# Performance work log

Measured on AMD Instinct MI355X. Metric: run time of the kernel, lower is better.

## Reference

```python
import jax, jax.numpy as jnp
import numpy as np

D_MODEL, D_STATE, D_CONV, EXPAND, HEADDIM = 256, 16, 4, 2, 16
D_INNER = EXPAND * D_MODEL            # 512
NHEADS = D_INNER // HEADDIM           # 32
CONV_DIM = D_INNER + 2 * D_STATE      # 544 (ngroups=1)
D_IN_PROJ = 2 * D_INNER + 2 * D_STATE + NHEADS  # 1088
BATCH, SEQLEN = 8, 4096


def setup_inputs() -> dict:
    key = jax.random.key(0)
    ks = jax.random.split(key, 8)
    u = jax.random.normal(ks[0], (BATCH, SEQLEN, D_MODEL), jnp.float32)
    W_in = jax.random.normal(ks[1], (D_MODEL, D_IN_PROJ), jnp.float32) * 0.02
    conv_w = jax.random.normal(ks[2], (CONV_DIM, 1, D_CONV), jnp.float32) * 0.2
    conv_b = jnp.zeros((CONV_DIM,), jnp.float32)
    # dt_bias init: inverse-softplus of dt ~ Uniform in log-space [dt_min, dt_max]
    dt = jnp.exp(jax.random.uniform(ks[3], (NHEADS,), jnp.float32)
                 * (np.log(0.1) - np.log(0.001)) + np.log(0.001))
    dt = jnp.clip(dt, 1e-4, None)
    dt_bias = dt + jnp.log(-jnp.expm1(-dt))
    A_log = jnp.log(jax.random.uniform(ks[4], (NHEADS,), jnp.float32, 1.0, 16.0))
    D = jnp.ones((NHEADS,), jnp.float32)
    norm_w = jnp.ones((D_INNER,), jnp.float32)
    W_out = jax.random.normal(ks[5], (D_INNER, D_MODEL), jnp.float32) * 0.02
    return dict(u=u, W_in=W_in, conv_w=conv_w, conv_b=conv_b, dt_bias=dt_bias,
                A_log=A_log, D=D, norm_w=norm_w, W_out=W_out)


def _mamba2_forward(u, W_in, conv_w, conv_b, dt_bias, A_log, D, norm_w, W_out):
    batch, seqlen, _ = u.shape
    zxbcdt = u @ W_in                                   # (B, L, 2*d_inner + 2*N + H)
    z = zxbcdt[..., :D_INNER]                           # gate
    xBC = zxbcdt[..., D_INNER:2 * D_INNER + 2 * D_STATE]
    dt = jax.nn.softplus(zxbcdt[..., -NHEADS:] + dt_bias)  # (B, L, H)
    # causal depthwise conv1d over time + SiLU
    xc = jnp.transpose(xBC, (0, 2, 1))                  # (B, C, L)
    xc = jax.lax.conv_general_dilated(
        xc, conv_w, window_strides=(1,), padding=[(D_CONV - 1, 0)],
        feature_group_count=CONV_DIM, dimension_numbers=('NCH', 'OIH', 'NCH'))
    xBC = jax.nn.silu(jnp.transpose(xc, (0, 2, 1)) + conv_b)
    x = xBC[..., :D_INNER].reshape(batch, seqlen, NHEADS, HEADDIM)  # (B,L,H,P)
    Bm = xBC[..., D_INNER:D_INNER + D_STATE]            # (B, L, N), ngroups=1
    Cm = xBC[..., D_INNER + D_STATE:]                   # (B, L, N)
    A = -jnp.exp(A_log)                                 # (H,)
    dA = jnp.exp(dt * A)                                # (B, L, H) decay per step

    # selective scan: h_t = dA_t * h_{t-1} + dt_t * (B_t outer x_t); y_t = C_t . h_t
    def step(h, inp):
        da_t, dt_t, b_t, x_t, c_t = inp
        h = da_t[:, :, None, None] * h + jnp.einsum('bh,bn,bhp->bhpn', dt_t, b_t, x_t)
        y_t = jnp.einsum('bhpn,bn->bhp', h, c_t)
        return h, y_t

    h0 = jnp.zeros((batch, NHEADS, HEADDIM, D_STATE), u.dtype)
    xs = (jnp.moveaxis(dA, 1, 0), jnp.moveaxis(dt, 1, 0),
          jnp.moveaxis(Bm, 1, 0), jnp.moveaxis(x, 1, 0), jnp.moveaxis(Cm, 1, 0))
    _, ys = jax.lax.scan(step, h0, xs)                  # ys: (L, B, H, P)
    y = jnp.moveaxis(ys, 0, 1) + D[None, None, :, None] * x
    y = y.reshape(batch, seqlen, D_INNER)
    # gated RMSNorm (norm_before_gate=False): normalize(y * silu(z)) * weight
    t = y * jax.nn.silu(z)
    t = t * jax.lax.rsqrt(jnp.mean(t * t, axis=-1, keepdims=True) + 1e-5) * norm_w
    return t @ W_out


def reference(u, W_in, conv_w, conv_b, dt_bias, A_log, D, norm_w, W_out):
    return _mamba2_forward(u, W_in, conv_w, conv_b, dt_bias, A_log, D, norm_w, W_out)
```

## Files before the change

### kernel.cpp

```cpp
#include <hip/hip_runtime.h>
#include <hip/hip_bf16.h>
#include <math.h>

#define BATCH   8
#define SEQLEN  4096
#define DMODEL  256
#define DSTATE  16
#define NHEADS  32
#define HEADDIM 16
#define DINNER  512
#define CONVDIM 544
#define DINPROJ 1088
#define NROWS   (BATCH*SEQLEN)
#define CHUNK   64
#define NCH     (SEQLEN/CHUNK)

typedef __attribute__((ext_vector_type(8))) short short8;
typedef __attribute__((ext_vector_type(8))) unsigned short ushort8;
typedef __attribute__((ext_vector_type(4))) float f32x4;

__device__ __forceinline__ float bfu2f(unsigned short u){
  union { float f; unsigned int i; } x; x.i = ((unsigned int)u) << 16; return x.f;
}
__device__ __forceinline__ unsigned short f2bfu(float f){
  union { float f; unsigned int u; } v; v.f = f;
  v.u += 0x7fffu + ((v.u >> 16) & 1u);
  return (unsigned short)(v.u >> 16);
}

__global__ __launch_bounds__(256) void k_cast_u(const float* __restrict__ u, unsigned short* __restrict__ ub){
  int i = blockIdx.x*256 + threadIdx.x;
  float4 v = reinterpret_cast<const float4*>(u)[i];
  ushort4 o; o.x=f2bfu(v.x); o.y=f2bfu(v.y); o.z=f2bfu(v.z); o.w=f2bfu(v.w);
  reinterpret_cast<ushort4*>(ub)[i] = o;
}

__global__ __launch_bounds__(256) void k_transpose_cast(const float* __restrict__ W, unsigned short* __restrict__ WT, int K, int N){
  int idx = blockIdx.x*256 + threadIdx.x;
  if (idx >= N*K) return;
  int n = idx / K, k = idx - n*K;
  WT[idx] = f2bfu(W[(size_t)k*N + n]);
}

template<int EPI, int WC, int K, int NYL2>
__global__ __launch_bounds__(WC*128) void k_gemm(
    const unsigned short* __restrict__ A,
    const unsigned short* __restrict__ BT,
    int nbase,
    unsigned short* __restrict__ oz,
    unsigned short* __restrict__ oxbc,
    float* __restrict__ odtraw,
    float* __restrict__ of32, int Nout)
{
  constexpr int BN = WC*32;
  constexpr int NAI = 4/WC;
  __shared__ uint4 lds[512 + BN*4];
  const int tid = threadIdx.x;
  const int l   = tid & 63;
  const int w   = tid >> 6;
  const int wr  = w & 1, wc = w >> 1;
  int bx, by;
  if (NYL2 == 0){ bx = blockIdx.x; by = 0; }
  else {
    int flat = blockIdx.x;
    int xcd = flat & 7;
    int grp = flat >> 3;
    by = grp & ((1 << NYL2) - 1);
    bx = (grp >> NYL2)*8 + xcd;
  }
  const int bm0 = bx * 128;
  const int bn0 = nbase + by * BN;
  const int fr  = l & 15, kq = l >> 4;
  f32x4 acc[4][2] = {};
  const int nK = K >> 5;
  for (int kt = 0; kt < nK; ++kt){
    const int k0 = kt << 5;
    #pragma unroll
    for (int i = 0; i < NAI; ++i){
      int c = tid + i*(WC*128);
      int row = c >> 2, slot = c & 3;
      uint4 v = *reinterpret_cast<const uint4*>(A + (size_t)(bm0+row)*K + k0 + slot*8);
      lds[row*4 + (slot ^ (row & 3))] = v;
    }
    {
      int row = tid >> 2, slot = tid & 3;
      uint4 v = *reinterpret_cast<const uint4*>(BT + (size_t)(bn0+row)*K + k0 + slot*8);
      lds[512 + row*4 + (slot ^ (row & 3))] = v;
    }
    __syncthreads();
    short8 bfrag[2];
    #pragma unroll
    for (int nf = 0; nf < 2; ++nf){
      int rb = wc*32 + nf*16 + fr;
      bfrag[nf] = *reinterpret_cast<const short8*>(&lds[512 + rb*4 + (kq ^ (rb & 3))]);
    }
    #pragma unroll
    for (int mf = 0; mf < 4; ++mf){
      int ra = wr*64 + mf*16 + fr;
      short8 afrag = *reinterpret_cast<const short8*>(&lds[ra*4 + (kq ^ (ra & 3))]);
      #pragma unroll
      for (int nf = 0; nf < 2; ++nf)
        acc[mf][nf] = __builtin_amdgcn_mfma_f32_16x16x32_bf16(afrag, bfrag[nf], acc[mf][nf], 0, 0, 0);
    }
    __syncthreads();
  }
  #pragma unroll
  for (int mf = 0; mf < 4; ++mf){
    #pragma unroll
    for (int nf = 0; nf < 2; ++nf){
      #pragma unroll
      for (int r = 0; r < 4; ++r){
        int m = bm0 + wr*64 + mf*16 + kq*4 + r;
        int n = bn0 + wc*32 + nf*16 + fr;
        float v = acc[mf][nf][r];
        if (EPI == 1){
          if (n < DINNER)                 oz[(size_t)m*DINNER + n] = f2bfu(v);
          else if (n < DINNER + CONVDIM)  oxbc[(size_t)m*CONVDIM + (n - DINNER)] = f2bfu(v);
          else                            odtraw[(size_t)m*NHEADS + (n - DINNER - CONVDIM)] = v;
        } else {
          of32[(size_t)m*Nout + n] = v;
        }
      }
    }
  }
}

__global__ __launch_bounds__(256) void k_convbc(const unsigned short* __restrict__ xbc,
                                                const float* __restrict__ cw,
                                                const float* __restrict__ cb,
                                                float* __restrict__ bco){
  const int tid = threadIdx.x;
  const int j = tid & 31;
  const int rt = tid >> 5;
  const int r0 = blockIdx.x*64 + rt*8;
  const int ch = 512 + j;
  const int tloc = r0 & (SEQLEN-1);
  float wv0 = cw[ch*4+0], wv1 = cw[ch*4+1], wv2 = cw[ch*4+2], wv3 = cw[ch*4+3];
  const float bias = cb[ch];
  float xr[11];
  #pragma unroll
  for (int k = 0; k < 11; ++k){
    int r = r0 - 3 + k;
    xr[k] = (tloc - 3 + k < 0) ? 0.f : bfu2f(xbc[(size_t)r*CONVDIM + ch]);
  }
  #pragma unroll
  for (int i = 0; i < 8; ++i){
    float acc = fmaf(wv0, xr[i], fmaf(wv1, xr[i+1], fmaf(wv2, xr[i+2], fmaf(wv3, xr[i+3], bias))));
    bco[(size_t)(r0+i)*32 + j] = acc / (1.f + __expf(-acc));
  }
}

__global__ __launch_bounds__(256) void k_dtda(const float* __restrict__ dtraw,
                                              const float* __restrict__ dt_bias,
                                              const float* __restrict__ A_log,
                                              float* __restrict__ dt_o,
                                              float* __restrict__ dA_o){
  int i = blockIdx.x*256 + threadIdx.x;
  int h = i & (NHEADS-1);
  float x = dtraw[i] + dt_bias[h];
  float dt = (x > 20.f) ? x : log1pf(expf(x));
  dt_o[i] = dt;
  dA_o[i] = expf(-expf(A_log[h]) * dt);
}

__global__ __launch_bounds__(256,4) void k_scan1(
    const unsigned short* __restrict__ xbc, const float* __restrict__ bc,
    const float* __restrict__ dta, const float* __restrict__ daa,
    const float* __restrict__ cwv, const float* __restrict__ cbv,
    const float* __restrict__ Dv,
    float* __restrict__ yl, float* __restrict__ st, float* __restrict__ Pp)
{
  __shared__ float sBC[65*32];
  __shared__ float sdt[65*16];
  __shared__ float sda[65*16];
  const int tid = threadIdx.x;
  const int bid = blockIdx.x;
  const int qh = bid & 1;
  const int c  = (bid >> 1) & (NCH-1);
  const int b  = bid >> 7;
  const int w  = tid >> 6;
  const int l  = tid & 63;
  const int q  = qh*4 + w;
  const int hh = l >> 4, p = l & 15;
  const int h  = q*4 + hh;
  const size_t row0 = (size_t)b*SEQLEN + (size_t)c*CHUNK;
  const int xoff = q*64 + l;
  {
    const float* src = bc + row0*32;
    #pragma unroll
    for (int i = 0; i < 2; ++i){
      int idx = tid + i*256;
      *reinterpret_cast<float4*>(&sBC[idx*4]) = *reinterpret_cast<const float4*>(src + (size_t)idx*4);
    }
  }
  {
    int t = tid >> 2, g = (tid & 3)*4;
    *reinterpret_cast<float4*>(&sdt[t*16+g]) =
      *reinterpret_cast<const float4*>(dta + (row0+t)*NHEADS + qh*16 + g);
    *reinterpret_cast<float4*>(&sda[t*16+g]) =
      *reinterpret_cast<const float4*>(daa + (row0+t)*NHEADS + qh*16 + g);
  }
  const float cw0 = cwv[xoff*4+0], cw1 = cwv[xoff*4+1], cw2 = cwv[xoff*4+2], cw3 = cwv[xoff*4+3];
  const float cb0 = cbv[xoff];
  const float Dh = Dv[h];
  const int dIdx = w*4 + hh;
  float wA, wB, wC;
  if (c == 0){ wA = wB = wC = 0.f; }
  else {
    wA = bfu2f(xbc[(row0-3)*CONVDIM + xoff]);
    wB = bfu2f(xbc[(row0-2)*CONVDIM + xoff]);
    wC = bfu2f(xbc[(row0-1)*CONVDIM + xoff]);
  }
  float xq0 = bfu2f(xbc[(row0+0)*CONVDIM + xoff]);
  float xq1 = bfu2f(xbc[(row0+1)*CONVDIM + xoff]);
  float xq2 = bfu2f(xbc[(row0+2)*CONVDIM + xoff]);
  float xq3 = bfu2f(xbc[(row0+3)*CONVDIM + xoff]);
  __syncthreads();
  float BA[32], BB[32];
  #pragma unroll
  for (int k = 0; k < 8; ++k)
    *reinterpret_cast<float4*>(&BA[4*k]) = *reinterpret_cast<const float4*>(&sBC[4*k]);
  float dtA = sdt[dIdx], daA = sda[dIdx];
  float dtB, daB;
  float hs[16];
  #pragma unroll
  for (int n = 0; n < 16; ++n) hs[n] = 0.f;
  float cum = 1.f;

#define S1STEP(CUR, NXT, DTC, DAC, DTN, DAN, XQ, T) {                          \
    const int t_ = (T);                                                        \
    _Pragma("unroll")                                                          \
    for (int k = 0; k < 8; ++k)                                                \
      *reinterpret_cast<float4*>(&NXT[4*k]) =                                  \
        *reinterpret_cast<const float4*>(&sBC[(t_+1)*32 + 4*k]);               \
    DTN = sdt[(t_+1)*16 + dIdx]; DAN = sda[(t_+1)*16 + dIdx];                  \
    float xnew = bfu2f(xbc[(row0 + t_ + 4)*CONVDIM + xoff]);                   \
    float xc = fmaf(cw0, wA, fmaf(cw1, wB, fmaf(cw2, wC, fmaf(cw3, XQ, cb0))));\
    wA = wB; wB = wC; wC = XQ; XQ = xnew;                                      \
    float xs = xc / (1.f + __expf(-xc));                                       \
    float dx = DTC * xs;                                                       \
    float y_ = 0.f;                                                            \
    _Pragma("unroll")                                                          \
    for (int n = 0; n < 16; ++n) hs[n] = fmaf(DAC, hs[n], dx*CUR[n]);          \
    _Pragma("unroll")                                                          \
    for (int n = 0; n < 16; ++n) y_ = fmaf(hs[n], CUR[16+n], y_);              \
    cum *= DAC;                                                                \
    yl[(row0 + t_)*DINNER + xoff] = y_ + Dh*xs;                                \
  }

  for (int T = 0; T < CHUNK; T += 4){
    S1STEP(BA, BB, dtA, daA, dtB, daB, xq0, T+0);
    S1STEP(BB, BA, dtB, daB, dtA, daA, xq1, T+1);
    S1STEP(BA, BB, dtA, daA, dtB, daB, xq2, T+2);
    S1STEP(BB, BA, dtB, daB, dtA, daA, xq3, T+3);
  }
#undef S1STEP
  float* sp = st + (((size_t)(b*NHEADS + h)*NCH + c)*16 + p)*16;
  #pragma unroll
  for (int k = 0; k < 4; ++k)
    *reinterpret_cast<float4*>(sp + 4*k) = make_float4(hs[4*k], hs[4*k+1], hs[4*k+2], hs[4*k+3]);
  if (p == 0) Pp[((size_t)b*NHEADS + h)*NCH + c] = cum;
}

__global__ __launch_bounds__(64) void k_scan2(float* __restrict__ st, const float* __restrict__ Pp){
  const int bh = blockIdx.x;
  const int l = threadIdx.x;
  float* sb = st + (size_t)bh*NCH*256 + l*4;
  const float* pb = Pp + (size_t)bh*NCH;
  float4 carry = make_float4(0.f,0.f,0.f,0.f);
  float4 Hb[4]; float Pb[4];
  #pragma unroll
  for (int i = 0; i < 4; ++i){
    Hb[i] = *reinterpret_cast<const float4*>(sb + (size_t)i*256);
    Pb[i] = pb[i];
  }
  for (int c0 = 0; c0 < NCH; c0 += 4){
    #pragma unroll
    for (int i = 0; i < 4; ++i){
      const int cc = c0 + i;
      float4 Hc = Hb[i]; float Pc = Pb[i];
      if (cc + 4 < NCH){
        Hb[i] = *reinterpret_cast<const float4*>(sb + (size_t)(cc+4)*256);
        Pb[i] = pb[cc+4];
      }
      *reinterpret_cast<float4*>(sb + (size_t)cc*256) = carry;
      carry.x = fmaf(Pc, carry.x, Hc.x);
      carry.y = fmaf(Pc, carry.y, Hc.y);
      carry.z = fmaf(Pc, carry.z, Hc.z);
      carry.w = fmaf(Pc, carry.w, Hc.w);
    }
  }
}

__global__ __launch_bounds__(256,4) void k_scan3(
    const float* __restrict__ yl, const float* __restrict__ bc,
    const float* __restrict__ daa, const float* __restrict__ st,
    unsigned short* __restrict__ ybf)
{
  __shared__ float sC[65*16];
  __shared__ float sda[65*16];
  const int tid = threadIdx.x;
  const int bid = blockIdx.x;
  const int qh = bid & 1;
  const int c  = (bid >> 1) & (NCH-1);
  const int b  = bid >> 7;
  const int w  = tid >> 6;
  const int l  = tid & 63;
  const int q  = qh*4 + w;
  const int hh = l >> 4, p = l & 15;
  const int h  = q*4 + hh;
  const size_t row0 = (size_t)b*SEQLEN + (size_t)c*CHUNK;
  const int xoff = q*64 + l;
  {
    int t = tid >> 2, g = (tid & 3)*4;
    *reinterpret_cast<float4*>(&sC[t*16+g]) =
      *reinterpret_cast<const float4*>(bc + (row0+t)*32 + 16 + g);
    *reinterpret_cast<float4*>(&sda[t*16+g]) =
      *reinterpret_cast<const float4*>(daa + (row0+t)*NHEADS + qh*16 + g);
  }
  float hi[16];
  {
    const float* sp = st + (((size_t)(b*NHEADS + h)*NCH + c)*16 + p)*16;
    #pragma unroll
    for (int k = 0; k < 4; ++k){
      float4 v = *reinterpret_cast<const float4*>(sp + 4*k);
      hi[4*k] = v.x; hi[4*k+1] = v.y; hi[4*k+2] = v.z; hi[4*k+3] = v.w;
    }
  }
  float yq0 = yl[(row0+0)*DINNER + xoff];
  float yq1 = yl[(row0+1)*DINNER + xoff];
  float yq2 = yl[(row0+2)*DINNER + xoff];
  float yq3 = yl[(row0+3)*DINNER + xoff];
  __syncthreads();
  const int dIdx = w*4 + hh;
  float CA[16], CB[16];
  #pragma unroll
  for (int k = 0; k < 4; ++k)
    *reinterpret_cast<float4*>(&CA[4*k]) = *reinterpret_cast<const float4*>(&sC[4*k]);
  float daA = sda[dIdx], daB;
  float cum = 1.f;

#define S3STEP(CUR, NXT, DAC, DAN, YQ, T) {                                    \
    const int t_ = (T);                                                        \
    _Pragma("unroll")                                                          \
    for (int k = 0; k < 4; ++k)                                                \
      *reinterpret_cast<float4*>(&NXT[4*k]) =                                  \
        *reinterpret_cast<const float4*>(&sC[(t_+1)*16 + 4*k]);                \
    DAN = sda[(t_+1)*16 + dIdx];                                               \
    float ynew = yl[(row0 + t_ + 4)*DINNER + xoff];                            \
    cum *= DAC;                                                                \
    float corr = 0.f;                                                          \
    _Pragma("unroll")                                                          \
    for (int n = 0; n < 16; ++n) corr = fmaf(hi[n], CUR[n], corr);             \
    ybf[(row0 + t_)*DINNER + xoff] = f2bfu(YQ + cum*corr);                     \
    YQ = ynew;                                                                 \
  }

  for (int T = 0; T < CHUNK; T += 4){
    S3STEP(CA, CB, daA, daB, yq0, T+0);
    S3STEP(CB, CA, daB, daA, yq1, T+1);
    S3STEP(CA, CB, daA, daB, yq2, T+2);
    S3STEP(CB, CA, daB, daA, yq3, T+3);
  }
#undef S3STEP
}

__global__ __launch_bounds__(256) void k_gate(const unsigned short* __restrict__ ybf,
                                              unsigned short* __restrict__ zbf,
                                              const float* __restrict__ nw){
  int row = blockIdx.x*4 + (threadIdx.x >> 6);
  int l = threadIdx.x & 63;
  size_t base = (size_t)row*DINNER + l*8;
  ushort8 yv = *reinterpret_cast<const ushort8*>(ybf + base);
  ushort8 zv = *reinterpret_cast<const ushort8*>(zbf + base);
  float tv[8]; float ss = 0.f;
  #pragma unroll
  for (int j = 0; j < 8; ++j){
    float yf = bfu2f(yv[j]);
    float zf = bfu2f(zv[j]);
    float s = zf / (1.f + __expf(-zf));
    float t = yf * s; tv[j] = t; ss += t*t;
  }
  #pragma unroll
  for (int m = 1; m <= 32; m <<= 1) ss += __shfl_xor(ss, m, 64);
  float scale = rsqrtf(ss * (1.f/DINNER) + 1e-5f);
  ushort8 o;
  #pragma unroll
  for (int j = 0; j < 8; ++j) o[j] = f2bfu(tv[j] * scale * nw[l*8+j]);
  *reinterpret_cast<ushort8*>(zbf + base) = o;
}

extern "C" void kernel_launch(void* const* d_in, const int* in_sizes, int n_in,
                              void* d_out, int out_size, void* d_ws, size_t ws_size,
                              hipStream_t stream)
{
  const float* u       = (const float*)d_in[0];
  const float* W_in    = (const float*)d_in[1];
  const float* conv_w  = (const float*)d_in[2];
  const float* conv_b  = (const float*)d_in[3];
  const float* dt_bias = (const float*)d_in[4];
  const float* A_log   = (const float*)d_in[5];
  const float* Dvec    = (const float*)d_in[6];
  const float* norm_w  = (const float*)d_in[7];
  const float* W_out   = (const float*)d_in[8];
  float* out = (float*)d_out;
  char* ws = (char*)d_ws;

  unsigned short* ubf   = (unsigned short*)(ws + 0);
  float* chst           = (float*)(ws + 0);
  unsigned short* wintT = (unsigned short*)(ws + 16777216);
  unsigned short* woutT = (unsigned short*)(ws + 17334272);
  unsigned short* zbf   = (unsigned short*)(ws + 17596416);
  unsigned short* xbcbf = (unsigned short*)(ws + 51150848);
  float* dtraw          = (float*)(ws + 86802432);
  float* Pp             = dtraw;
  float* ylocal         = (float*)(ws + 90996736);
  float* convoBC        = (float*)(ws + 158105600);
  float* dtq            = (float*)(ws + 162299904);
  float* daq            = (float*)(ws + 166494208);
  unsigned short* ybf   = xbcbf;

  k_cast_u<<<NROWS*DMODEL/1024, 256, 0, stream>>>(u, ubf);
  k_transpose_cast<<<(DINPROJ*DMODEL+255)/256, 256, 0, stream>>>(W_in, wintT, DMODEL, DINPROJ);
  k_transpose_cast<<<(DINNER*DMODEL+255)/256, 256, 0, stream>>>(W_out, woutT, DINNER, DMODEL);

  k_gemm<1,4,DMODEL,3><<<(NROWS/128)*8, 512, 0, stream>>>(ubf, wintT, 0, zbf, xbcbf, dtraw, nullptr, 0);
  k_gemm<1,2,DMODEL,0><<<NROWS/128, 256, 0, stream>>>(ubf, wintT, 1024, zbf, xbcbf, dtraw, nullptr, 0);

  k_convbc<<<NROWS/64, 256, 0, stream>>>(xbcbf, conv_w, conv_b, convoBC);
  k_dtda<<<NROWS*NHEADS/256, 256, 0, stream>>>(dtraw, dt_bias, A_log, dtq, daq);

  k_scan1<<<BATCH*2*NCH, 256, 0, stream>>>(xbcbf, convoBC, dtq, daq, conv_w, conv_b, Dvec,
                                           ylocal, chst, Pp);
  k_scan2<<<BATCH*NHEADS, 64, 0, stream>>>(chst, Pp);
  k_scan3<<<BATCH*2*NCH, 256, 0, stream>>>(ylocal, convoBC, daq, chst, ybf);

  k_gate<<<NROWS/4, 256, 0, stream>>>(ybf, zbf, norm_w);

  k_gemm<2,4,DINNER,1><<<(NROWS/128)*2, 512, 0, stream>>>(zbf, woutT, 0, nullptr, nullptr, nullptr, out, DMODEL);
}
```

Measured before the change: 177.0 us.

## Fuse gated RMSNorm into scan3 and deepen x prefetch in scan1

Folds the gated RMSNorm kernel into the chunk-scan output pass. Each block now covers all 512 channels of a chunk with 512 threads, so the per-row sum of squares can be reduced through shuffles plus a small shared buffer, and the normalized result is written straight into zbf. This removes the bf16 y round trip through global memory and one kernel launch, at the cost of a block barrier every four timesteps and half as many blocks. Separately, scan1 now prefetches the conv input eight steps ahead instead of four, to hide more global load latency.

Result: slower. 240.3 us (+35.7%).

```diff
diff --git a/kernel.cpp b/kernel.cpp
--- a/kernel.cpp
+++ b/kernel.cpp
@@ -215,6 +215,10 @@
   float xq1 = bfu2f(xbc[(row0+1)*CONVDIM + xoff]);
   float xq2 = bfu2f(xbc[(row0+2)*CONVDIM + xoff]);
   float xq3 = bfu2f(xbc[(row0+3)*CONVDIM + xoff]);
+  float xq4 = bfu2f(xbc[(row0+4)*CONVDIM + xoff]);
+  float xq5 = bfu2f(xbc[(row0+5)*CONVDIM + xoff]);
+  float xq6 = bfu2f(xbc[(row0+6)*CONVDIM + xoff]);
+  float xq7 = bfu2f(xbc[(row0+7)*CONVDIM + xoff]);
   __syncthreads();
   float BA[32], BB[32];
   #pragma unroll
@@ -234,7 +238,7 @@
       *reinterpret_cast<float4*>(&NXT[4*k]) =                                  \
         *reinterpret_cast<const float4*>(&sBC[(t_+1)*32 + 4*k]);               \
     DTN = sdt[(t_+1)*16 + dIdx]; DAN = sda[(t_+1)*16 + dIdx];                  \
-    float xnew = bfu2f(xbc[(row0 + t_ + 4)*CONVDIM + xoff]);                   \
+    float xnew = bfu2f(xbc[(row0 + t_ + 8)*CONVDIM + xoff]);                   \
     float xc = fmaf(cw0, wA, fmaf(cw1, wB, fmaf(cw2, wC, fmaf(cw3, XQ, cb0))));\
     wA = wB; wB = wC; wC = XQ; XQ = xnew;                                      \
     float xs = xc / (1.f + __expf(-xc));                                       \
@@ -248,11 +252,15 @@
     yl[(row0 + t_)*DINNER + xoff] = y_ + Dh*xs;                                \
   }
 
-  for (int T = 0; T < CHUNK; T += 4){
+  for (int T = 0; T < CHUNK; T += 8){
     S1STEP(BA, BB, dtA, daA, dtB, daB, xq0, T+0);
     S1STEP(BB, BA, dtB, daB, dtA, daA, xq1, T+1);
     S1STEP(BA, BB, dtA, daA, dtB, daB, xq2, T+2);
     S1STEP(BB, BA, dtB, daB, dtA, daA, xq3, T+3);
+    S1STEP(BA, BB, dtA, daA, dtB, daB, xq4, T+4);
+    S1STEP(BB, BA, dtB, daB, dtA, daA, xq5, T+5);
+    S1STEP(BA, BB, dtA, daA, dtB, daB, xq6, T+6);
+    S1STEP(BB, BA, dtB, daB, dtA, daA, xq7, T+7);
   }
 #undef S1STEP
   float* sp = st + (((size_t)(b*NHEADS + h)*NCH + c)*16 + p)*16;
@@ -292,31 +300,37 @@
   }
 }
 
-__global__ __launch_bounds__(256,4) void k_scan3(
+__global__ __launch_bounds__(512) void k_scan3g(
     const float* __restrict__ yl, const float* __restrict__ bc,
     const float* __restrict__ daa, const float* __restrict__ st,
-    unsigned short* __restrict__ ybf)
+    unsigned short* __restrict__ zbf, const float* __restrict__ nw)
 {
   __shared__ float sC[65*16];
-  __shared__ float sda[65*16];
+  __shared__ float sda[65*32];
+  __shared__ float sred[2][4][8];
   const int tid = threadIdx.x;
   const int bid = blockIdx.x;
-  const int qh = bid & 1;
-  const int c  = (bid >> 1) & (NCH-1);
-  const int b  = bid >> 7;
-  const int w  = tid >> 6;
-  const int l  = tid & 63;
-  const int q  = qh*4 + w;
+  const int c = bid & (NCH-1);
+  const int b = bid >> 6;
+  const int w = tid >> 6;
+  const int l = tid & 63;
   const int hh = l >> 4, p = l & 15;
-  const int h  = q*4 + hh;
+  const int h = w*4 + hh;
   const size_t row0 = (size_t)b*SEQLEN + (size_t)c*CHUNK;
-  const int xoff = q*64 + l;
-  {
+  const int xoff = w*64 + l;
+  if (tid < 256){
     int t = tid >> 2, g = (tid & 3)*4;
     *reinterpret_cast<float4*>(&sC[t*16+g]) =
       *reinterpret_cast<const float4*>(bc + (row0+t)*32 + 16 + g);
-    *reinterpret_cast<float4*>(&sda[t*16+g]) =
-      *reinterpret_cast<const float4*>(daa + (row0+t)*NHEADS + qh*16 + g);
+  } else {
+    int j = tid - 256;
+    #pragma unroll
+    for (int kk = 0; kk < 2; ++kk){
+      int idx = j*2 + kk;
+      int t = idx >> 3, g = (idx & 7)*4;
+      *reinterpret_cast<float4*>(&sda[t*32+g]) =
+        *reinterpret_cast<const float4*>(daa + (row0+t)*NHEADS + g);
+    }
   }
   float hi[16];
   {
@@ -327,67 +341,75 @@
       hi[4*k] = v.x; hi[4*k+1] = v.y; hi[4*k+2] = v.z; hi[4*k+3] = v.w;
     }
   }
+  const float nwv = nw[xoff];
   float yq0 = yl[(row0+0)*DINNER + xoff];
   float yq1 = yl[(row0+1)*DINNER + xoff];
   float yq2 = yl[(row0+2)*DINNER + xoff];
   float yq3 = yl[(row0+3)*DINNER + xoff];
+  float zq0 = bfu2f(zbf[(row0+0)*DINNER + xoff]);
+  float zq1 = bfu2f(zbf[(row0+1)*DINNER + xoff]);
+  float zq2 = bfu2f(zbf[(row0+2)*DINNER + xoff]);
+  float zq3 = bfu2f(zbf[(row0+3)*DINNER + xoff]);
   __syncthreads();
-  const int dIdx = w*4 + hh;
   float CA[16], CB[16];
   #pragma unroll
   for (int k = 0; k < 4; ++k)
     *reinterpret_cast<float4*>(&CA[4*k]) = *reinterpret_cast<const float4*>(&sC[4*k]);
-  float daA = sda[dIdx], daB;
+  float daA = sda[h], daB;
   float cum = 1.f;
 
-#define S3STEP(CUR, NXT, DAC, DAN, YQ, T) {                                    \
+#define S3STEP(CUR, NXT, DAC, DAN, YQ, ZQ, TV, PS, T) {                        \
     const int t_ = (T);                                                        \
     _Pragma("unroll")                                                          \
     for (int k = 0; k < 4; ++k)                                                \
       *reinterpret_cast<float4*>(&NXT[4*k]) =                                  \
         *reinterpret_cast<const float4*>(&sC[(t_+1)*16 + 4*k]);                \
-    DAN = sda[(t_+1)*16 + dIdx];                                               \
+    DAN = sda[(t_+1)*32 + h];                                                  \
     float ynew = yl[(row0 + t_ + 4)*DINNER + xoff];                            \
+    float znew = bfu2f(zbf[(row0 + t_ + 4)*DINNER + xoff]);                    \
     cum *= DAC;                                                                \
     float corr = 0.f;                                                          \
     _Pragma("unroll")                                                          \
     for (int n = 0; n < 16; ++n) corr = fmaf(hi[n], CUR[n], corr);             \
-    ybf[(row0 + t_)*DINNER + xoff] = f2bfu(YQ + cum*corr);                     \
-    YQ = ynew;                                                                 \
+    float yv = YQ + cum*corr;                                                  \
+    float sg = ZQ / (1.f + __expf(-ZQ));                                       \
+    TV = yv * sg; PS = TV*TV;                                                  \
+    YQ = ynew; ZQ = znew;                                                      \
   }
 
   for (int T = 0; T < CHUNK; T += 4){
-    S3STEP(CA, CB, daA, daB, yq0, T+0);
-    S3STEP(CB, CA, daB, daA, yq1, T+1);
-    S3STEP(CA, CB, daA, daB, yq2, T+2);
-    S3STEP(CB, CA, daB, daA, yq3, T+3);
+    float tv0, tv1, tv2, tv3, ps0, ps1, ps2, ps3;
+    S3STEP(CA, CB, daA, daB, yq0, zq0, tv0, ps0, T+0);
+    S3STEP(CB, CA, daB, daA, yq1, zq1, tv1, ps1, T+1);
+    S3STEP(CA, CB, daA, daB, yq2, zq2, tv2, ps2, T+2);
+    S3STEP(CB, CA, daB, daA, yq3, zq3, tv3, ps3, T+3);
+    #pragma unroll
+    for (int m = 1; m <= 32; m <<= 1){
+      ps0 += __shfl_xor(ps0, m, 64);
+      ps1 += __shfl_xor(ps1, m, 64);
+      ps2 += __shfl_xor(ps2, m, 64);
+      ps3 += __shfl_xor(ps3, m, 64);
+    }
+    const int gb = (T >> 2) & 1;
+    if (l == 0){
+      sred[gb][0][w] = ps0; sred[gb][1][w] = ps1;
+      sred[gb][2][w] = ps2; sred[gb][3][w] = ps3;
+    }
+    __syncthreads();
+    float ss[4];
+    #pragma unroll
+    for (int i = 0; i < 4; ++i){
+      float4 ra = *reinterpret_cast<const float4*>(&sred[gb][i][0]);
+      float4 rb = *reinterpret_cast<const float4*>(&sred[gb][i][4]);
+      ss[i] = (ra.x+ra.y)+(ra.z+ra.w)+((rb.x+rb.y)+(rb.z+rb.w));
+    }
+    unsigned short* zp = zbf + (row0 + T)*DINNER + xoff;
+    zp[0*DINNER] = f2bfu(tv0 * rsqrtf(ss[0]*(1.f/DINNER) + 1e-5f) * nwv);
+    zp[1*DINNER] = f2bfu(tv1 * rsqrtf(ss[1]*(1.f/DINNER) + 1e-5f) * nwv);
+    zp[2*DINNER] = f2bfu(tv2 * rsqrtf(ss[2]*(1.f/DINNER) + 1e-5f) * nwv);
+    zp[3*DINNER] = f2bfu(tv3 * rsqrtf(ss[3]*(1.f/DINNER) + 1e-5f) * nwv);
   }
 #undef S3STEP
-}
-
-__global__ __launch_bounds__(256) void k_gate(const unsigned short* __restrict__ ybf,
-                                              unsigned short* __restrict__ zbf,
-                                              const float* __restrict__ nw){
-  int row = blockIdx.x*4 + (threadIdx.x >> 6);
-  int l = threadIdx.x & 63;
-  size_t base = (size_t)row*DINNER + l*8;
-  ushort8 yv = *reinterpret_cast<const ushort8*>(ybf + base);
-  ushort8 zv = *reinterpret_cast<const ushort8*>(zbf + base);
-  float tv[8]; float ss = 0.f;
-  #pragma unroll
-  for (int j = 0; j < 8; ++j){
-    float yf = bfu2f(yv[j]);
-    float zf = bfu2f(zv[j]);
-    float s = zf / (1.f + __expf(-zf));
-    float t = yf * s; tv[j] = t; ss += t*t;
-  }
-  #pragma unroll
-  for (int m = 1; m <= 32; m <<= 1) ss += __shfl_xor(ss, m, 64);
-  float scale = rsqrtf(ss * (1.f/DINNER) + 1e-5f);
-  ushort8 o;
-  #pragma unroll
-  for (int j = 0; j < 8; ++j) o[j] = f2bfu(tv[j] * scale * nw[l*8+j]);
-  *reinterpret_cast<ushort8*>(zbf + base) = o;
 }
 
 extern "C" void kernel_launch(void* const* d_in, const int* in_sizes, int n_in,
@@ -418,7 +440,6 @@
   float* convoBC        = (float*)(ws + 158105600);
   float* dtq            = (float*)(ws + 162299904);
   float* daq            = (float*)(ws + 166494208);
-  unsigned short* ybf   = xbcbf;
 
   k_cast_u<<<NROWS*DMODEL/1024, 256, 0, stream>>>(u, ubf);
   k_transpose_cast<<<(DINPROJ*DMODEL+255)/256, 256, 0, stream>>>(W_in, wintT, DMODEL, DINPROJ);
@@ -433,9 +454,7 @@
   k_scan1<<<BATCH*2*NCH, 256, 0, stream>>>(xbcbf, convoBC, dtq, daq, conv_w, conv_b, Dvec,
                                            ylocal, chst, Pp);
   k_scan2<<<BATCH*NHEADS, 64, 0, stream>>>(chst, Pp);
-  k_scan3<<<BATCH*2*NCH, 256, 0, stream>>>(ylocal, convoBC, daq, chst, ybf);
-
-  k_gate<<<NROWS/4, 256, 0, stream>>>(ybf, zbf, norm_w);
+  k_scan3g<<<BATCH*NCH, 512, 0, stream>>>(ylocal, convoBC, daq, chst, zbf, norm_w);
 
   k_gemm<2,4,DINNER,1><<<(NROWS/128)*2, 512, 0, stream>>>(zbf, woutT, 0, nullptr, nullptr, nullptr, out, DMODEL);
 }
```
